# Optimization experiments

Hardware: AMD Instinct MI355X
Metric: run time of the kernel (lower is better)

Reference implementation:

```python
import jax, jax.numpy as jnp
import numpy as np

D_MODEL = 512
NHEAD = 4
HEAD_DIM = D_MODEL // NHEAD


def setup_inputs() -> dict:
    key = jax.random.key(0)
    ks = jax.random.split(key, 12)
    B, S = 2, 4096
    s = 1.0 / np.sqrt(D_MODEL)
    inp = {
        "query": jax.random.normal(ks[0], (B, S, D_MODEL), jnp.float32),
        "key": jax.random.normal(ks[1], (B, S, D_MODEL), jnp.float32),
        "value": jax.random.normal(ks[2], (B, S, D_MODEL), jnp.float32),
        "Wq": jax.random.uniform(ks[3], (D_MODEL, D_MODEL), jnp.float32, -s, s),
        "bq": jax.random.uniform(ks[4], (D_MODEL,), jnp.float32, -s, s),
        "Wk": jax.random.uniform(ks[5], (D_MODEL, D_MODEL), jnp.float32, -s, s),
        "bk": jax.random.uniform(ks[6], (D_MODEL,), jnp.float32, -s, s),
        "Wv": jax.random.uniform(ks[7], (D_MODEL, D_MODEL), jnp.float32, -s, s),
        "bv": jax.random.uniform(ks[8], (D_MODEL,), jnp.float32, -s, s),
        "Wo": jax.random.uniform(ks[9], (D_MODEL, D_MODEL), jnp.float32, -s, s),
        "bo": jax.random.uniform(ks[10], (D_MODEL,), jnp.float32, -s, s),
    }
    return inp


def reference(query, key, value, Wq, bq, Wk, bk, Wv, bv, Wo, bo):
    B, Sq, _ = query.shape
    Sk = key.shape[1]
    # projections (torch Linear: x @ W.T + b); split heads -> [B, H, S, hd]
    def proj(x, W, b, S):
        return (x @ W.T + b).reshape(B, S, NHEAD, HEAD_DIM).transpose(0, 2, 1, 3)
    Q = proj(query, Wq, bq, Sq)
    K = proj(key, Wk, bk, Sk)
    V = proj(value, Wv, bv, Sk)
    scale = 1.0 / np.sqrt(HEAD_DIM).astype(np.float32)
    scores = jnp.einsum("bhqd,bhkd->bhqk", Q, K) * scale  # [B,H,Sq,Sk]
    weights = jax.nn.softmax(scores, axis=-1)
    out = jnp.einsum("bhqk,bhkd->bhqd", weights, V)  # [B,H,Sq,hd]
    out = out.transpose(0, 2, 1, 3).reshape(B, Sq, D_MODEL)
    return out @ Wo.T + bo
```

## Files before the change

### kernel.cpp

```cpp
#include <hip/hip_runtime.h>


#define D_MODEL 512
#define NHEAD 4
#define HD 128
#define S_ 4096

typedef __attribute__((ext_vector_type(8))) short bf16x8;
typedef __attribute__((ext_vector_type(4))) short bf16x4;
typedef __attribute__((ext_vector_type(4))) float f32x4;
typedef __attribute__((ext_vector_type(2))) unsigned uint2v;
typedef __attribute__((ext_vector_type(4))) unsigned uint4v;

#define SCQ (0.08838834764831845f * 1.4426950408889634f)

__device__ __forceinline__ short f2bf(float f) {
    unsigned u = __builtin_bit_cast(unsigned, f);
    u += 0x7fffu + ((u >> 16) & 1u);
    return (short)(u >> 16);
}
__device__ __forceinline__ unsigned pk2bf(float a, float b) {
    unsigned ua = __builtin_bit_cast(unsigned, a);
    ua += 0x7fffu + ((ua >> 16) & 1u);
    unsigned ub = __builtin_bit_cast(unsigned, b);
    ub += 0x7fffu + ((ub >> 16) & 1u);
    return (ua >> 16) | (ub & 0xffff0000u);
}
__device__ __forceinline__ void gl2lds16(const short* g, short* l) {
    __builtin_amdgcn_global_load_lds(
        (const __attribute__((address_space(1))) void*)g,
        (__attribute__((address_space(3))) void*)l, 16, 0, 0);
}

__global__ __launch_bounds__(256) void convert_kernel(
    const float* __restrict__ s0, const float* __restrict__ s1,
    const float* __restrict__ s2, const float* __restrict__ s3,
    const float* __restrict__ s4, const float* __restrict__ s5,
    const float* __restrict__ s6,
    short* __restrict__ d0, short* __restrict__ d1, short* __restrict__ d2,
    short* __restrict__ d3, short* __restrict__ d4, short* __restrict__ d5,
    short* __restrict__ d6)
{
    int seg = blockIdx.y;
    const float* src; short* dst; int n;
    const int NBIG = 2 * S_ * D_MODEL;
    const int NW = D_MODEL * D_MODEL;
    switch (seg) {
        case 0: src = s0; dst = d0; n = NBIG; break;
        case 1: src = s1; dst = d1; n = NBIG; break;
        case 2: src = s2; dst = d2; n = NBIG; break;
        case 3: src = s3; dst = d3; n = NW; break;
        case 4: src = s4; dst = d4; n = NW; break;
        case 5: src = s5; dst = d5; n = NW; break;
        default: src = s6; dst = d6; n = NW; break;
    }
    int idx = (blockIdx.x * 256 + threadIdx.x) * 8;
    if (idx >= n) return;
    float4 a = *(const float4*)(src + idx);
    float4 b = *(const float4*)(src + idx + 4);
    uint4v o;
    o[0] = pk2bf(a.x, a.y); o[1] = pk2bf(a.z, a.w);
    o[2] = pk2bf(b.x, b.y); o[3] = pk2bf(b.z, b.w);
    *(uint4v*)(dst + idx) = o;
}

__global__ __launch_bounds__(256) void qkv_kernel(
    const short* __restrict__ qb, const short* __restrict__ kb,
    const short* __restrict__ vb,
    const short* __restrict__ Wqb, const short* __restrict__ Wkb,
    const short* __restrict__ Wvb,
    const float* __restrict__ bq, const float* __restrict__ bk,
    const float* __restrict__ bv,
    short* __restrict__ Qh, short* __restrict__ Kh, short* __restrict__ VT)
{
    __shared__ short smem[24576];
    int z = blockIdx.z;
    const short* A    = (z == 0) ? qb  : (z == 1) ? kb  : vb;
    const short* W    = (z == 0) ? Wqb : (z == 1) ? Wkb : Wvb;
    const float* bias = (z == 0) ? bq  : (z == 1) ? bk  : bv;
    short* out        = (z == 0) ? Qh  : (z == 1) ? Kh  : VT;
    int vmode = (z == 2);
    float osc = (z == 0) ? SCQ : 1.0f;

    int t = threadIdx.x;
    int wv = t >> 6, ln = t & 63, q4 = ln >> 4, c = ln & 15;
    int m0 = blockIdx.x * 64, n0 = blockIdx.y * 128;
    f32x4 acc[8] = {};

    {
        short* lAd = smem;
        short* lBd = smem + 8192;
        #pragma unroll
        for (int i = 0; i < 2; ++i) {
            int id = i * 256 + t;
            int m = id >> 3, kgp = id & 7;
            gl2lds16(A + (size_t)(m0 + m) * 512 + ((kgp ^ (m & 7)) << 3), &lAd[id * 8]);
        }
        #pragma unroll
        for (int i = 0; i < 4; ++i) {
            int id = i * 256 + t;
            int n = id >> 3, kgp = id & 7;
            gl2lds16(W + (size_t)(n0 + n) * 512 + ((kgp ^ (n & 7)) << 3), &lBd[id * 8]);
        }
    }
    asm volatile("s_waitcnt vmcnt(0)" ::: "memory");
    __builtin_amdgcn_s_barrier();
    __builtin_amdgcn_sched_barrier(0);

    int cur = 0;
    for (int k0 = 0; k0 < 512; k0 += 64) {
        int more = (k0 < 448);
        if (more) {
            short* lAd = smem + (cur ^ 1) * 4096;
            short* lBd = smem + 8192 + (cur ^ 1) * 8192;
            int kn = k0 + 64;
            #pragma unroll
            for (int i = 0; i < 2; ++i) {
                int id = i * 256 + t;
                int m = id >> 3, kgp = id & 7;
                gl2lds16(A + (size_t)(m0 + m) * 512 + kn + ((kgp ^ (m & 7)) << 3), &lAd[id * 8]);
            }
            #pragma unroll
            for (int i = 0; i < 4; ++i) {
                int id = i * 256 + t;
                int n = id >> 3, kgp = id & 7;
                gl2lds16(W + (size_t)(n0 + n) * 512 + kn + ((kgp ^ (n & 7)) << 3), &lBd[id * 8]);
            }
        }
        short* lAc = smem + cur * 4096;
        short* lBc = smem + 8192 + cur * 8192;
        __builtin_amdgcn_s_setprio(1);
        #pragma unroll
        for (int ks = 0; ks < 2; ++ks) {
            int kg = ks * 4 + q4;
            int m = wv * 16 + c;
            bf16x8 af = *(bf16x8*)&lAc[m * 64 + ((kg ^ (m & 7)) << 3)];
            bf16x8 bfr[8];
            #pragma unroll
            for (int nt = 0; nt < 8; ++nt) {
                int n = nt * 16 + c;
                bfr[nt] = *(bf16x8*)&lBc[n * 64 + ((kg ^ (n & 7)) << 3)];
            }
            #pragma unroll
            for (int nt = 0; nt < 8; ++nt)
                acc[nt] = __builtin_amdgcn_mfma_f32_16x16x32_bf16(af, bfr[nt], acc[nt], 0, 0, 0);
        }
        __builtin_amdgcn_s_setprio(0);
        if (more) asm volatile("s_waitcnt vmcnt(0)" ::: "memory");
        __builtin_amdgcn_s_barrier();
        __builtin_amdgcn_sched_barrier(0);
        cur ^= 1;
    }

    if (vmode == 0) {
        const int TS = 136;
        short* lT = smem;
        for (int nt = 0; nt < 8; ++nt) {
            float bv_ = bias[n0 + nt * 16 + c];
            for (int r = 0; r < 4; ++r) {
                int srow = wv * 16 + q4 * 4 + r;
                lT[srow * TS + nt * 16 + c] = f2bf((acc[nt][r] + bv_) * osc);
            }
        }
        __syncthreads();
        int bb = m0 >> 12, sbase = m0 & 4095, h = blockIdx.y;
        for (int i = 0; i < 4; ++i) {
            int id = i * 256 + t;
            int row = id >> 4, g = id & 15;
            bf16x8 vv = *(bf16x8*)&lT[row * TS + g * 8];
            *(bf16x8*)&out[((size_t)((bb * NHEAD + h) * S_ + sbase + row)) * HD + g * 8] = vv;
        }
    } else {
        short* lB0 = smem + 8192;
        for (int nt = 0; nt < 8; ++nt) {
            int d = nt * 16 + c;
            float bv_ = bias[n0 + d];
            uint2v pv;
            pv[0] = pk2bf(acc[nt][0] + bv_, acc[nt][1] + bv_);
            pv[1] = pk2bf(acc[nt][2] + bv_, acc[nt][3] + bv_);
            int gr = wv * 4 + q4;
            *(uint2v*)&lB0[d * 64 + ((gr ^ (d & 15)) << 2)] = pv;
        }
        __syncthreads();
        int bb = m0 >> 12, sbase = m0 & 4095, h = blockIdx.y;
        for (int i = 0; i < 8; ++i) {
            int id = i * 256 + t;
            int d = id >> 4, grl = id & 15;
            bf16x4 v = *(bf16x4*)&lB0[d * 64 + ((grl ^ (d & 15)) << 2)];
            *(bf16x4*)&out[((size_t)((bb * NHEAD + h) * HD + d)) * S_ + sbase + grl * 4] = v;
        }
    }
}

__global__ __launch_bounds__(256) void outproj_kernel(
    const short* __restrict__ A, const short* __restrict__ W,
    const float* __restrict__ bias, float* __restrict__ out)
{
    __shared__ short smem[24576];
    int t = threadIdx.x;
    int wv = t >> 6, ln = t & 63, q4 = ln >> 4, c = ln & 15;
    int m0 = blockIdx.x * 64, n0 = blockIdx.y * 128;
    f32x4 acc[8] = {};

    {
        short* lAd = smem;
        short* lBd = smem + 8192;
        #pragma unroll
        for (int i = 0; i < 2; ++i) {
            int id = i * 256 + t;
            int m = id >> 3, kgp = id & 7;
            gl2lds16(A + (size_t)(m0 + m) * 512 + ((kgp ^ (m & 7)) << 3), &lAd[id * 8]);
        }
        #pragma unroll
        for (int i = 0; i < 4; ++i) {
            int id = i * 256 + t;
            int n = id >> 3, kgp = id & 7;
            gl2lds16(W + (size_t)(n0 + n) * 512 + ((kgp ^ (n & 7)) << 3), &lBd[id * 8]);
        }
    }
    asm volatile("s_waitcnt vmcnt(0)" ::: "memory");
    __builtin_amdgcn_s_barrier();
    __builtin_amdgcn_sched_barrier(0);

    int cur = 0;
    for (int k0 = 0; k0 < 512; k0 += 64) {
        int more = (k0 < 448);
        if (more) {
            short* lAd = smem + (cur ^ 1) * 4096;
            short* lBd = smem + 8192 + (cur ^ 1) * 8192;
            int kn = k0 + 64;
            #pragma unroll
            for (int i = 0; i < 2; ++i) {
                int id = i * 256 + t;
                int m = id >> 3, kgp = id & 7;
                gl2lds16(A + (size_t)(m0 + m) * 512 + kn + ((kgp ^ (m & 7)) << 3), &lAd[id * 8]);
            }
            #pragma unroll
            for (int i = 0; i < 4; ++i) {
                int id = i * 256 + t;
                int n = id >> 3, kgp = id & 7;
                gl2lds16(W + (size_t)(n0 + n) * 512 + kn + ((kgp ^ (n & 7)) << 3), &lBd[id * 8]);
            }
        }
        short* lAc = smem + cur * 4096;
        short* lBc = smem + 8192 + cur * 8192;
        __builtin_amdgcn_s_setprio(1);
        #pragma unroll
        for (int ks = 0; ks < 2; ++ks) {
            int kg = ks * 4 + q4;
            int m = wv * 16 + c;
            bf16x8 af = *(bf16x8*)&lAc[m * 64 + ((kg ^ (m & 7)) << 3)];
            bf16x8 bfr[8];
            #pragma unroll
            for (int nt = 0; nt < 8; ++nt) {
                int n = nt * 16 + c;
                bfr[nt] = *(bf16x8*)&lBc[n * 64 + ((kg ^ (n & 7)) << 3)];
            }
            #pragma unroll
            for (int nt = 0; nt < 8; ++nt)
                acc[nt] = __builtin_amdgcn_mfma_f32_16x16x32_bf16(af, bfr[nt], acc[nt], 0, 0, 0);
        }
        __builtin_amdgcn_s_setprio(0);
        if (more) asm volatile("s_waitcnt vmcnt(0)" ::: "memory");
        __builtin_amdgcn_s_barrier();
        __builtin_amdgcn_sched_barrier(0);
        cur ^= 1;
    }

    for (int nt = 0; nt < 8; ++nt) {
        int col = n0 + nt * 16 + c;
        float bv_ = bias[col];
        for (int r = 0; r < 4; ++r) {
            int mrow = m0 + wv * 16 + q4 * 4 + r;
            out[(size_t)mrow * 512 + col] = acc[nt][r] + bv_;
        }
    }
}

__device__ __forceinline__ void stage_k(const short* __restrict__ Kh, size_t base,
                                        int kk, short* dst, int t) {
    #pragma unroll
    for (int i = 0; i < 4; ++i) {
        int id = i * 256 + t;
        int m = id >> 4, kgp = id & 15;
        gl2lds16(Kh + base + (size_t)(kk + m) * HD + ((kgp ^ (m & 7)) << 3), &dst[id * 8]);
    }
}
__device__ __forceinline__ void stage_vt(const short* __restrict__ VTg, size_t base,
                                         int kk, short* dst, int t) {
    #pragma unroll
    for (int i = 0; i < 4; ++i) {
        int id = i * 256 + t;
        int mv = id >> 3, kgvp = id & 7;
        gl2lds16(VTg + base + (size_t)mv * S_ + kk + ((kgvp ^ (mv & 7)) << 3), &dst[id * 8]);
    }
}
__device__ __forceinline__ void qk_tile(const short* kb, const bf16x8 (&qf)[2][4],
                                        int q4, int c, f32x4 (&sf)[2][4]) {
    #pragma unroll
    for (int ks = 0; ks < 4; ++ks) {
        int kg = ks * 4 + q4;
        bf16x8 af[4];
        #pragma unroll
        for (int kt = 0; kt < 4; ++kt) {
            int row = kt * 16 + c;
            af[kt] = *(bf16x8*)&kb[row * 128 + ((kg ^ (row & 7)) << 3)];
        }
        #pragma unroll
        for (int qt = 0; qt < 2; ++qt)
            #pragma unroll
            for (int kt = 0; kt < 4; ++kt)
                sf[qt][kt] = __builtin_amdgcn_mfma_f32_16x16x32_bf16(
                    af[kt], qf[qt][ks], sf[qt][kt], 0, 0, 0);
    }
}
__device__ __forceinline__ void pv_tile(const short* vb, const bf16x8 (&bp)[2][2],
                                        int q4, int c, f32x4 (&of)[8][2]) {
    #pragma unroll
    for (int ksv = 0; ksv < 2; ++ksv) {
        int kg = ksv * 4 + q4;
        bf16x8 av[8];
        #pragma unroll
        for (int dt = 0; dt < 8; ++dt) {
            int row = dt * 16 + c;
            av[dt] = *(bf16x8*)&vb[row * 64 + ((kg ^ (row & 7)) << 3)];
        }
        #pragma unroll
        for (int qt = 0; qt < 2; ++qt)
            #pragma unroll
            for (int dt = 0; dt < 8; ++dt)
                of[dt][qt] = __builtin_amdgcn_mfma_f32_16x16x32_bf16(
                    av[dt], bp[qt][ksv], of[dt][qt], 0, 0, 0);
    }
}
__device__ __forceinline__ void sm_tile(const f32x4 (&sf)[2][4], float (&lrun)[2],
                                        bf16x8 (&bp)[2][2]) {
    #pragma unroll
    for (int qt = 0; qt < 2; ++qt) {
        unsigned dlo[4], dhi[4];
        float lt = 0.f;
        #pragma unroll
        for (int kt = 0; kt < 4; ++kt) {
            float p0 = exp2f(sf[qt][kt][0]);
            float p1 = exp2f(sf[qt][kt][1]);
            float p2 = exp2f(sf[qt][kt][2]);
            float p3 = exp2f(sf[qt][kt][3]);
            lt += (p0 + p1) + (p2 + p3);
            asm("v_cvt_pk_bf16_f32 %0, %1, %2" : "=v"(dlo[kt]) : "v"(p0), "v"(p1));
            asm("v_cvt_pk_bf16_f32 %0, %1, %2" : "=v"(dhi[kt]) : "v"(p2), "v"(p3));
        }
        lrun[qt] += lt;
        #pragma unroll
        for (int ksv = 0; ksv < 2; ++ksv) {
            unsigned x0 = dlo[2 * ksv], y0 = dlo[2 * ksv + 1];
            unsigned x1 = dhi[2 * ksv], y1 = dhi[2 * ksv + 1];
            asm("v_permlane32_swap_b32 %0, %1" : "+v"(x0), "+v"(y0));
            asm("v_permlane16_swap_b32 %0, %1" : "+v"(x0), "+v"(y0));
            asm("v_permlane32_swap_b32 %0, %1" : "+v"(x1), "+v"(y1));
            asm("v_permlane16_swap_b32 %0, %1" : "+v"(x1), "+v"(y1));
            uint4v u; u[0] = x0; u[1] = x1; u[2] = y0; u[3] = y1;
            bp[qt][ksv] = __builtin_bit_cast(bf16x8, u);
        }
    }
}

#define FLASH_BAR() do { \
    asm volatile("s_waitcnt vmcnt(0)" ::: "memory"); \
    __builtin_amdgcn_s_barrier(); \
    __builtin_amdgcn_sched_barrier(0); } while (0)

__global__ __launch_bounds__(256, 2) void flash_kernel(
    const short* __restrict__ Qh, const short* __restrict__ Kh,
    const short* __restrict__ VTg, short* __restrict__ AO,
    float* __restrict__ U, float* __restrict__ ML, int nsplit, int kkspan)
{
    __shared__ short lK[2][64 * 128];
    __shared__ short lVT[2][128 * 64];
    int t = threadIdx.x;
    int wv = t >> 6, ln = t & 63, q4 = ln >> 4, c = ln & 15;
    int bh = blockIdx.x;
    int s0 = blockIdx.y * 128;
    int z = blockIdx.z;
    const size_t base = (size_t)bh * S_ * HD;

    bf16x8 qf[2][4];
    #pragma unroll
    for (int qt = 0; qt < 2; ++qt) {
        int s = s0 + wv * 32 + qt * 16 + c;
        const short* qp = Qh + base + (size_t)s * HD + q4 * 8;
        #pragma unroll
        for (int ks = 0; ks < 4; ++ks)
            qf[qt][ks] = *(const bf16x8*)(qp + ks * 32);
    }

    f32x4 of[8][2] = {};
    float lrun[2] = {};
    bf16x8 bpA[2][2], bpB[2][2];

    int kkbeg = z * kkspan;
    int ntl = kkspan >> 6;

    stage_k(Kh, base, kkbeg, &lK[0][0], t);
    FLASH_BAR();

    {
        stage_k(Kh, base, kkbeg + 64, &lK[1][0], t);
        stage_vt(VTg, base, kkbeg, &lVT[0][0], t);
        f32x4 sf[2][4] = {};
        __builtin_amdgcn_s_setprio(1);
        qk_tile(&lK[0][0], qf, q4, c, sf);
        __builtin_amdgcn_s_setprio(0);
        sm_tile(sf, lrun, bpA);
        FLASH_BAR();
    }

    for (int j = 1; j + 1 < ntl; j += 2) {
        {
            int kk0 = kkbeg + j * 64;
            stage_k(Kh, base, kk0 + 64, &lK[0][0], t);
            stage_vt(VTg, base, kk0, &lVT[1][0], t);
            f32x4 sf[2][4] = {};
            __builtin_amdgcn_s_setprio(1);
            qk_tile(&lK[1][0], qf, q4, c, sf);
            pv_tile(&lVT[0][0], bpA, q4, c, of);
            __builtin_amdgcn_s_setprio(0);
            sm_tile(sf, lrun, bpB);
            FLASH_BAR();
        }
        {
            int kk0 = kkbeg + (j + 1) * 64;
            if (j + 2 < ntl) stage_k(Kh, base, kk0 + 64, &lK[1][0], t);
            stage_vt(VTg, base, kk0, &lVT[0][0], t);
            f32x4 sf[2][4] = {};
            __builtin_amdgcn_s_setprio(1);
            qk_tile(&lK[0][0], qf, q4, c, sf);
            pv_tile(&lVT[1][0], bpB, q4, c, of);
            __builtin_amdgcn_s_setprio(0);
            sm_tile(sf, lrun, bpA);
            FLASH_BAR();
        }
    }

    {
        int kk0 = kkbeg + (ntl - 1) * 64;
        stage_vt(VTg, base, kk0, &lVT[1][0], t);
        f32x4 sf[2][4] = {};
        __builtin_amdgcn_s_setprio(1);
        qk_tile(&lK[1][0], qf, q4, c, sf);
        pv_tile(&lVT[0][0], bpA, q4, c, of);
        __builtin_amdgcn_s_setprio(0);
        sm_tile(sf, lrun, bpB);
        FLASH_BAR();
    }

    __builtin_amdgcn_s_setprio(1);
    pv_tile(&lVT[1][0], bpB, q4, c, of);
    __builtin_amdgcn_s_setprio(0);

    #pragma unroll
    for (int qt = 0; qt < 2; ++qt) {
        lrun[qt] += __shfl_xor(lrun[qt], 16);
        lrun[qt] += __shfl_xor(lrun[qt], 32);
    }

    if (nsplit > 1) {
        #pragma unroll
        for (int qt = 0; qt < 2; ++qt) {
            int s = s0 + wv * 32 + qt * 16 + c;
            size_t rowu = (size_t)(z * 8 + bh) * S_ + s;
            float* up = U + rowu * HD;
            #pragma unroll
            for (int dt = 0; dt < 8; ++dt)
                *(f32x4*)&up[dt * 16 + q4 * 4] = of[dt][qt];
            if (q4 == 0) ML[rowu] = lrun[qt];
        }
    } else {
        int b = bh >> 2, h = bh & 3;
        #pragma unroll
        for (int qt = 0; qt < 2; ++qt) {
            float inv = 1.0f / lrun[qt];
            int s = s0 + wv * 32 + qt * 16 + c;
            short* dst = AO + ((size_t)(b * S_ + s)) * D_MODEL + h * HD;
            #pragma unroll
            for (int dt = 0; dt < 8; ++dt) {
                uint2v ov;
                ov[0] = pk2bf(of[dt][qt][0] * inv, of[dt][qt][1] * inv);
                ov[1] = pk2bf(of[dt][qt][2] * inv, of[dt][qt][3] * inv);
                *(uint2v*)(dst + dt * 16 + q4 * 4) = ov;
            }
        }
    }
}

__global__ __launch_bounds__(256) void combine_kernel(
    const float* __restrict__ U, const float* __restrict__ ML,
    short* __restrict__ AO, int nsplit)
{
    int row = blockIdx.x * 8 + (threadIdx.x >> 5);
    int d4 = (threadIdx.x & 31) * 4;
    const int R = 8 * S_;
    float l = 0.f;
    f32x4 u = {0.f, 0.f, 0.f, 0.f};
    for (int zz = 0; zz < nsplit; ++zz) {
        l += ML[(size_t)zz * R + row];
        f32x4 uz = *(const f32x4*)&U[((size_t)zz * R + row) * HD + d4];
        u += uz;
    }
    float inv = 1.0f / l;
    uint2v o;
    o[0] = pk2bf(u[0] * inv, u[1] * inv);
    o[1] = pk2bf(u[2] * inv, u[3] * inv);
    int bh = row >> 12, s = row & 4095;
    int b = bh >> 2, h = bh & 3;
    *(uint2v*)&AO[((size_t)(b * S_ + s)) * D_MODEL + h * HD + d4] = o;
}

extern "C" void kernel_launch(void* const* d_in, const int* in_sizes, int n_in,
                              void* d_out, int out_size, void* d_ws, size_t ws_size,
                              hipStream_t stream) {
    const float* q  = (const float*)d_in[0];
    const float* k  = (const float*)d_in[1];
    const float* v  = (const float*)d_in[2];
    const float* Wq = (const float*)d_in[3];
    const float* bq = (const float*)d_in[4];
    const float* Wk = (const float*)d_in[5];
    const float* bk = (const float*)d_in[6];
    const float* Wv = (const float*)d_in[7];
    const float* bv = (const float*)d_in[8];
    const float* Wo = (const float*)d_in[9];
    const float* bo = (const float*)d_in[10];

    const size_t HS = (size_t)2 * NHEAD * S_ * HD;
    const size_t NBIG = HS;
    const size_t NW = (size_t)D_MODEL * D_MODEL;
    const size_t R = (size_t)8 * S_;

    char* wsb = (char*)d_ws;
    short* Qh = (short*)wsb;
    short* Kh = Qh + HS;
    short* VT = Kh + HS;
    short* AO = VT + HS;
    char* r2 = wsb + 4 * HS * 2;
    short* qb  = (short*)r2;
    short* kb  = qb + NBIG;
    short* vb  = kb + NBIG;
    short* Wqb = vb + NBIG;
    short* Wkb = Wqb + NW;
    short* Wvb = Wkb + NW;
    float* U   = (float*)r2;

    int nsplit = 1;
    size_t r2sz = 3 * NBIG * 2 + 3 * NW * 2;
    {
        int cand = 2;
        size_t r2c = (size_t)cand * R * HD * 4;
        if (r2c < 3 * NBIG * 2 + 3 * NW * 2) r2c = 3 * NBIG * 2 + 3 * NW * 2;
        size_t need = 4 * HS * 2 + r2c + (size_t)cand * R * 4 + NW * 2;
        if (ws_size >= need) { nsplit = cand; r2sz = r2c; }
    }
    float* ML  = (float*)(r2 + r2sz);
    short* Wob = (short*)((char*)ML + (size_t)nsplit * R * 4);
    int kkspan = S_ / nsplit;

    dim3 blk(256);
    convert_kernel<<<dim3(2048, 7), blk, 0, stream>>>(
        q, k, v, Wq, Wk, Wv, Wo, qb, kb, vb, Wqb, Wkb, Wvb, Wob);
    qkv_kernel<<<dim3(128, 4, 3), blk, 0, stream>>>(
        qb, kb, vb, Wqb, Wkb, Wvb, bq, bk, bv, Qh, Kh, VT);
    flash_kernel<<<dim3(8, 32, nsplit), blk, 0, stream>>>(
        Qh, Kh, VT, AO, U, ML, nsplit, kkspan);
    if (nsplit > 1)
        combine_kernel<<<dim3(S_), blk, 0, stream>>>(U, ML, AO, nsplit);
    outproj_kernel<<<dim3(128, 4), blk, 0, stream>>>(AO, Wob, bo, (float*)d_out);
}
```

Before: 228.8 us.

## Fuse activation bf16 conversion into QKV GEMM and split-combine into out-projection

The QKV projection now reads fp32 activations directly, converts them to bf16 in registers and writes them into swizzled LDS, so the large activation conversion pass and its intermediate buffers go away; the convert kernel now only handles the weights. The out-projection A-tile fetch now merges the two flash split partials and normalizes them inline, which removes the separate combine kernel and the AO round trip. The cost is that the A loads become register-staged rather than direct global-to-LDS loads, adding VGPR pressure and fp32 traffic inside the GEMMs. The split-combine path also reads twice as many fp32 bytes per A tile and recomputes it for each of the 4 N-blocks.

After: 230.9 us. About the same (+0.9%).

```diff
diff --git a/kernel.cpp b/kernel.cpp
--- a/kernel.cpp
+++ b/kernel.cpp
@@ -26,6 +26,12 @@
     ub += 0x7fffu + ((ub >> 16) & 1u);
     return (ua >> 16) | (ub & 0xffff0000u);
 }
+__device__ __forceinline__ uint4v pk8(float4 a, float4 b) {
+    uint4v o;
+    o[0] = pk2bf(a.x, a.y); o[1] = pk2bf(a.z, a.w);
+    o[2] = pk2bf(b.x, b.y); o[3] = pk2bf(b.z, b.w);
+    return o;
+}
 __device__ __forceinline__ void gl2lds16(const short* g, short* l) {
     __builtin_amdgcn_global_load_lds(
         (const __attribute__((address_space(1))) void*)g,
@@ -35,38 +41,21 @@
 __global__ __launch_bounds__(256) void convert_kernel(
     const float* __restrict__ s0, const float* __restrict__ s1,
     const float* __restrict__ s2, const float* __restrict__ s3,
-    const float* __restrict__ s4, const float* __restrict__ s5,
-    const float* __restrict__ s6,
-    short* __restrict__ d0, short* __restrict__ d1, short* __restrict__ d2,
-    short* __restrict__ d3, short* __restrict__ d4, short* __restrict__ d5,
-    short* __restrict__ d6)
+    short* __restrict__ d0, short* __restrict__ d1,
+    short* __restrict__ d2, short* __restrict__ d3)
 {
     int seg = blockIdx.y;
-    const float* src; short* dst; int n;
-    const int NBIG = 2 * S_ * D_MODEL;
-    const int NW = D_MODEL * D_MODEL;
-    switch (seg) {
-        case 0: src = s0; dst = d0; n = NBIG; break;
-        case 1: src = s1; dst = d1; n = NBIG; break;
-        case 2: src = s2; dst = d2; n = NBIG; break;
-        case 3: src = s3; dst = d3; n = NW; break;
-        case 4: src = s4; dst = d4; n = NW; break;
-        case 5: src = s5; dst = d5; n = NW; break;
-        default: src = s6; dst = d6; n = NW; break;
-    }
+    const float* src = (seg == 0) ? s0 : (seg == 1) ? s1 : (seg == 2) ? s2 : s3;
+    short* dst       = (seg == 0) ? d0 : (seg == 1) ? d1 : (seg == 2) ? d2 : d3;
     int idx = (blockIdx.x * 256 + threadIdx.x) * 8;
-    if (idx >= n) return;
     float4 a = *(const float4*)(src + idx);
     float4 b = *(const float4*)(src + idx + 4);
-    uint4v o;
-    o[0] = pk2bf(a.x, a.y); o[1] = pk2bf(a.z, a.w);
-    o[2] = pk2bf(b.x, b.y); o[3] = pk2bf(b.z, b.w);
-    *(uint4v*)(dst + idx) = o;
+    *(uint4v*)(dst + idx) = pk8(a, b);
 }
 
 __global__ __launch_bounds__(256) void qkv_kernel(
-    const short* __restrict__ qb, const short* __restrict__ kb,
-    const short* __restrict__ vb,
+    const float* __restrict__ qf32, const float* __restrict__ kf32,
+    const float* __restrict__ vf32,
     const short* __restrict__ Wqb, const short* __restrict__ Wkb,
     const short* __restrict__ Wvb,
     const float* __restrict__ bq, const float* __restrict__ bk,
@@ -75,10 +64,10 @@
 {
     __shared__ short smem[24576];
     int z = blockIdx.z;
-    const short* A    = (z == 0) ? qb  : (z == 1) ? kb  : vb;
-    const short* W    = (z == 0) ? Wqb : (z == 1) ? Wkb : Wvb;
-    const float* bias = (z == 0) ? bq  : (z == 1) ? bk  : bv;
-    short* out        = (z == 0) ? Qh  : (z == 1) ? Kh  : VT;
+    const float* A    = (z == 0) ? qf32 : (z == 1) ? kf32 : vf32;
+    const short* W    = (z == 0) ? Wqb  : (z == 1) ? Wkb  : Wvb;
+    const float* bias = (z == 0) ? bq   : (z == 1) ? bk   : bv;
+    short* out        = (z == 0) ? Qh   : (z == 1) ? Kh   : VT;
     int vmode = (z == 2);
     float osc = (z == 0) ? SCQ : 1.0f;
 
@@ -87,15 +76,18 @@
     int m0 = blockIdx.x * 64, n0 = blockIdx.y * 128;
     f32x4 acc[8] = {};
 
+    int mA0 = t >> 3, kg0 = t & 7;
+    int mA1 = 32 + (t >> 3), kg1 = t & 7;
+    const float* a0p = A + (size_t)(m0 + mA0) * 512 + kg0 * 8;
+    const float* a1p = A + (size_t)(m0 + mA1) * 512 + kg1 * 8;
+    int sw0 = mA0 * 64 + ((kg0 ^ (mA0 & 7)) << 3);
+    int sw1 = mA1 * 64 + ((kg1 ^ (mA1 & 7)) << 3);
+    float4 pa00, pa01, pa10, pa11;
+
+    pa00 = *(const float4*)(a0p);     pa01 = *(const float4*)(a0p + 4);
+    pa10 = *(const float4*)(a1p);     pa11 = *(const float4*)(a1p + 4);
     {
-        short* lAd = smem;
         short* lBd = smem + 8192;
-        #pragma unroll
-        for (int i = 0; i < 2; ++i) {
-            int id = i * 256 + t;
-            int m = id >> 3, kgp = id & 7;
-            gl2lds16(A + (size_t)(m0 + m) * 512 + ((kgp ^ (m & 7)) << 3), &lAd[id * 8]);
-        }
         #pragma unroll
         for (int i = 0; i < 4; ++i) {
             int id = i * 256 + t;
@@ -104,6 +96,9 @@
         }
     }
     asm volatile("s_waitcnt vmcnt(0)" ::: "memory");
+    *(uint4v*)&smem[sw0] = pk8(pa00, pa01);
+    *(uint4v*)&smem[sw1] = pk8(pa10, pa11);
+    asm volatile("s_waitcnt lgkmcnt(0)" ::: "memory");
     __builtin_amdgcn_s_barrier();
     __builtin_amdgcn_sched_barrier(0);
 
@@ -111,15 +106,10 @@
     for (int k0 = 0; k0 < 512; k0 += 64) {
         int more = (k0 < 448);
         if (more) {
-            short* lAd = smem + (cur ^ 1) * 4096;
+            int kn = k0 + 64;
+            pa00 = *(const float4*)(a0p + kn); pa01 = *(const float4*)(a0p + kn + 4);
+            pa10 = *(const float4*)(a1p + kn); pa11 = *(const float4*)(a1p + kn + 4);
             short* lBd = smem + 8192 + (cur ^ 1) * 8192;
-            int kn = k0 + 64;
-            #pragma unroll
-            for (int i = 0; i < 2; ++i) {
-                int id = i * 256 + t;
-                int m = id >> 3, kgp = id & 7;
-                gl2lds16(A + (size_t)(m0 + m) * 512 + kn + ((kgp ^ (m & 7)) << 3), &lAd[id * 8]);
-            }
             #pragma unroll
             for (int i = 0; i < 4; ++i) {
                 int id = i * 256 + t;
@@ -146,7 +136,13 @@
                 acc[nt] = __builtin_amdgcn_mfma_f32_16x16x32_bf16(af, bfr[nt], acc[nt], 0, 0, 0);
         }
         __builtin_amdgcn_s_setprio(0);
-        if (more) asm volatile("s_waitcnt vmcnt(0)" ::: "memory");
+        if (more) {
+            asm volatile("s_waitcnt vmcnt(0)" ::: "memory");
+            short* lAd = smem + (cur ^ 1) * 4096;
+            *(uint4v*)&lAd[sw0] = pk8(pa00, pa01);
+            *(uint4v*)&lAd[sw1] = pk8(pa10, pa11);
+        }
+        asm volatile("s_waitcnt lgkmcnt(0)" ::: "memory");
         __builtin_amdgcn_s_barrier();
         __builtin_amdgcn_sched_barrier(0);
         cur ^= 1;
@@ -193,8 +189,9 @@
 }
 
 __global__ __launch_bounds__(256) void outproj_kernel(
-    const short* __restrict__ A, const short* __restrict__ W,
-    const float* __restrict__ bias, float* __restrict__ out)
+    const short* __restrict__ AO, const float* __restrict__ U,
+    const float* __restrict__ ML, const short* __restrict__ W,
+    const float* __restrict__ bias, float* __restrict__ out, int nsplit)
 {
     __shared__ short smem[24576];
     int t = threadIdx.x;
@@ -202,15 +199,42 @@
     int m0 = blockIdx.x * 64, n0 = blockIdx.y * 128;
     f32x4 acc[8] = {};
 
+    int mA0 = t >> 3, kg0 = t & 7;
+    int mA1 = 32 + (t >> 3), kg1 = t & 7;
+    int g0row = m0 + mA0, g1row = m0 + mA1;
+    int b0 = g0row >> 12, s0r = g0row & 4095;
+    int b1 = g1row >> 12, s1r = g1row & 4095;
+    int sw0 = mA0 * 64 + ((kg0 ^ (mA0 & 7)) << 3);
+    int sw1 = mA1 * 64 + ((kg1 ^ (mA1 & 7)) << 3);
+    uint4v va0, va1;
+
+    auto fetchA = [&](int k0, int b, int srow, int kg, uint4v& dst) {
+        if (nsplit > 1) {
+            int bh = b * 4 + (k0 >> 7);
+            size_t r0 = (size_t)bh * S_ + srow;
+            size_t r1 = (size_t)(8 + bh) * S_ + srow;
+            const float* u0 = U + r0 * HD + (k0 & 127) + kg * 8;
+            const float* u1 = U + r1 * HD + (k0 & 127) + kg * 8;
+            float4 x0 = *(const float4*)(u0);
+            float4 x1 = *(const float4*)(u0 + 4);
+            float4 y0 = *(const float4*)(u1);
+            float4 y1 = *(const float4*)(u1 + 4);
+            float inv = 1.0f / (ML[r0] + ML[r1]);
+            uint4v o;
+            o[0] = pk2bf((x0.x + y0.x) * inv, (x0.y + y0.y) * inv);
+            o[1] = pk2bf((x0.z + y0.z) * inv, (x0.w + y0.w) * inv);
+            o[2] = pk2bf((x1.x + y1.x) * inv, (x1.y + y1.y) * inv);
+            o[3] = pk2bf((x1.z + y1.z) * inv, (x1.w + y1.w) * inv);
+            dst = o;
+        } else {
+            dst = *(const uint4v*)(AO + (size_t)(b * S_ + srow) * D_MODEL + k0 + kg * 8);
+        }
+    };
+
+    fetchA(0, b0, s0r, kg0, va0);
+    fetchA(0, b1, s1r, kg1, va1);
     {
-        short* lAd = smem;
         short* lBd = smem + 8192;
-        #pragma unroll
-        for (int i = 0; i < 2; ++i) {
-            int id = i * 256 + t;
-            int m = id >> 3, kgp = id & 7;
-            gl2lds16(A + (size_t)(m0 + m) * 512 + ((kgp ^ (m & 7)) << 3), &lAd[id * 8]);
-        }
         #pragma unroll
         for (int i = 0; i < 4; ++i) {
             int id = i * 256 + t;
@@ -219,6 +243,9 @@
         }
     }
     asm volatile("s_waitcnt vmcnt(0)" ::: "memory");
+    *(uint4v*)&smem[sw0] = va0;
+    *(uint4v*)&smem[sw1] = va1;
+    asm volatile("s_waitcnt lgkmcnt(0)" ::: "memory");
     __builtin_amdgcn_s_barrier();
     __builtin_amdgcn_sched_barrier(0);
 
@@ -226,15 +253,10 @@
     for (int k0 = 0; k0 < 512; k0 += 64) {
         int more = (k0 < 448);
         if (more) {
-            short* lAd = smem + (cur ^ 1) * 4096;
+            int kn = k0 + 64;
+            fetchA(kn, b0, s0r, kg0, va0);
+            fetchA(kn, b1, s1r, kg1, va1);
             short* lBd = smem + 8192 + (cur ^ 1) * 8192;
-            int kn = k0 + 64;
-            #pragma unroll
-            for (int i = 0; i < 2; ++i) {
-                int id = i * 256 + t;
-                int m = id >> 3, kgp = id & 7;
-                gl2lds16(A + (size_t)(m0 + m) * 512 + kn + ((kgp ^ (m & 7)) << 3), &lAd[id * 8]);
-            }
             #pragma unroll
             for (int i = 0; i < 4; ++i) {
                 int id = i * 256 + t;
@@ -261,7 +283,13 @@
                 acc[nt] = __builtin_amdgcn_mfma_f32_16x16x32_bf16(af, bfr[nt], acc[nt], 0, 0, 0);
         }
         __builtin_amdgcn_s_setprio(0);
-        if (more) asm volatile("s_waitcnt vmcnt(0)" ::: "memory");
+        if (more) {
+            asm volatile("s_waitcnt vmcnt(0)" ::: "memory");
+            short* lAd = smem + (cur ^ 1) * 4096;
+            *(uint4v*)&lAd[sw0] = va0;
+            *(uint4v*)&lAd[sw1] = va1;
+        }
+        asm volatile("s_waitcnt lgkmcnt(0)" ::: "memory");
         __builtin_amdgcn_s_barrier();
         __builtin_amdgcn_sched_barrier(0);
         cur ^= 1;
@@ -490,29 +518,6 @@
             }
         }
     }
-}
-
-__global__ __launch_bounds__(256) void combine_kernel(
-    const float* __restrict__ U, const float* __restrict__ ML,
-    short* __restrict__ AO, int nsplit)
-{
-    int row = blockIdx.x * 8 + (threadIdx.x >> 5);
-    int d4 = (threadIdx.x & 31) * 4;
-    const int R = 8 * S_;
-    float l = 0.f;
-    f32x4 u = {0.f, 0.f, 0.f, 0.f};
-    for (int zz = 0; zz < nsplit; ++zz) {
-        l += ML[(size_t)zz * R + row];
-        f32x4 uz = *(const f32x4*)&U[((size_t)zz * R + row) * HD + d4];
-        u += uz;
-    }
-    float inv = 1.0f / l;
-    uint2v o;
-    o[0] = pk2bf(u[0] * inv, u[1] * inv);
-    o[1] = pk2bf(u[2] * inv, u[3] * inv);
-    int bh = row >> 12, s = row & 4095;
-    int b = bh >> 2, h = bh & 3;
-    *(uint2v*)&AO[((size_t)(b * S_ + s)) * D_MODEL + h * HD + d4] = o;
 }
 
 extern "C" void kernel_launch(void* const* d_in, const int* in_sizes, int n_in,
@@ -531,45 +536,33 @@
     const float* bo = (const float*)d_in[10];
 
     const size_t HS = (size_t)2 * NHEAD * S_ * HD;
-    const size_t NBIG = HS;
     const size_t NW = (size_t)D_MODEL * D_MODEL;
     const size_t R = (size_t)8 * S_;
 
-    char* wsb = (char*)d_ws;
-    short* Qh = (short*)wsb;
-    short* Kh = Qh + HS;
-    short* VT = Kh + HS;
-    short* AO = VT + HS;
-    char* r2 = wsb + 4 * HS * 2;
-    short* qb  = (short*)r2;
-    short* kb  = qb + NBIG;
-    short* vb  = kb + NBIG;
-    short* Wqb = vb + NBIG;
+    short* Qh  = (short*)d_ws;
+    short* Kh  = Qh + HS;
+    short* VT  = Kh + HS;
+    short* AO  = VT + HS;
+    short* Wqb = AO + HS;
     short* Wkb = Wqb + NW;
     short* Wvb = Wkb + NW;
-    float* U   = (float*)r2;
+    short* Wob = Wvb + NW;
+    size_t fixed = 4 * HS * 2 + 4 * NW * 2;
 
     int nsplit = 1;
-    size_t r2sz = 3 * NBIG * 2 + 3 * NW * 2;
-    {
-        int cand = 2;
-        size_t r2c = (size_t)cand * R * HD * 4;
-        if (r2c < 3 * NBIG * 2 + 3 * NW * 2) r2c = 3 * NBIG * 2 + 3 * NW * 2;
-        size_t need = 4 * HS * 2 + r2c + (size_t)cand * R * 4 + NW * 2;
-        if (ws_size >= need) { nsplit = cand; r2sz = r2c; }
-    }
-    float* ML  = (float*)(r2 + r2sz);
-    short* Wob = (short*)((char*)ML + (size_t)nsplit * R * 4);
+    size_t need2 = fixed + (size_t)2 * R * HD * 4 + (size_t)2 * R * 4;
+    if (ws_size >= need2) nsplit = 2;
+    float* U  = (float*)((char*)d_ws + fixed);
+    float* ML = (float*)((char*)U + (size_t)nsplit * R * HD * 4);
     int kkspan = S_ / nsplit;
 
     dim3 blk(256);
-    convert_kernel<<<dim3(2048, 7), blk, 0, stream>>>(
-        q, k, v, Wq, Wk, Wv, Wo, qb, kb, vb, Wqb, Wkb, Wvb, Wob);
+    convert_kernel<<<dim3(128, 4), blk, 0, stream>>>(
+        Wq, Wk, Wv, Wo, Wqb, Wkb, Wvb, Wob);
     qkv_kernel<<<dim3(128, 4, 3), blk, 0, stream>>>(
-        qb, kb, vb, Wqb, Wkb, Wvb, bq, bk, bv, Qh, Kh, VT);
+        q, k, v, Wqb, Wkb, Wvb, bq, bk, bv, Qh, Kh, VT);
     flash_kernel<<<dim3(8, 32, nsplit), blk, 0, stream>>>(
         Qh, Kh, VT, AO, U, ML, nsplit, kkspan);
-    if (nsplit > 1)
-        combine_kernel<<<dim3(S_), blk, 0, stream>>>(U, ML, AO, nsplit);
-    outproj_kernel<<<dim3(128, 4), blk, 0, stream>>>(AO, Wob, bo, (float*)d_out);
-}
+    outproj_kernel<<<dim3(128, 4), blk, 0, stream>>>(
+        AO, U, ML, Wob, bo, (float*)d_out, nsplit);
+}
```

## Enlarge QKV projection tile to 128x128 with 2x2 warp layout

Applied to the files above, without the earlier changes.

The QKV GEMM block tile grows from 64x128 to 128x128, with the four warps arranged 2x2 so each computes a 64x64 sub-tile using 4x4 MFMA accumulators. This raises operand reuse per LDS load and halves the number of blocks that reload the weight tiles. The V-transpose epilogue now uses a padded LDS layout and 16-byte stores instead of swizzled 8-byte ones. The costs are more LDS per block (64 KB) and more accumulator registers, and the grid shrinks to 768 blocks, which may lower occupancy.

Result: no change. 229.1 us (+0.2%).

```diff
diff --git a/kernel.cpp b/kernel.cpp
--- a/kernel.cpp
+++ b/kernel.cpp
@@ -73,7 +73,7 @@
     const float* __restrict__ bv,
     short* __restrict__ Qh, short* __restrict__ Kh, short* __restrict__ VT)
 {
-    __shared__ short smem[24576];
+    __shared__ short smem[32768];
     int z = blockIdx.z;
     const short* A    = (z == 0) ? qb  : (z == 1) ? kb  : vb;
     const short* W    = (z == 0) ? Wqb : (z == 1) ? Wkb : Wvb;
@@ -84,23 +84,19 @@
 
     int t = threadIdx.x;
     int wv = t >> 6, ln = t & 63, q4 = ln >> 4, c = ln & 15;
-    int m0 = blockIdx.x * 64, n0 = blockIdx.y * 128;
-    f32x4 acc[8] = {};
+    int wi = wv >> 1, wj = wv & 1;
+    int m0 = blockIdx.x * 128, n0 = blockIdx.y * 128;
+    f32x4 acc[4][4] = {};
 
     {
         short* lAd = smem;
-        short* lBd = smem + 8192;
-        #pragma unroll
-        for (int i = 0; i < 2; ++i) {
+        short* lBd = smem + 16384;
+        #pragma unroll
+        for (int i = 0; i < 4; ++i) {
             int id = i * 256 + t;
             int m = id >> 3, kgp = id & 7;
             gl2lds16(A + (size_t)(m0 + m) * 512 + ((kgp ^ (m & 7)) << 3), &lAd[id * 8]);
-        }
-        #pragma unroll
-        for (int i = 0; i < 4; ++i) {
-            int id = i * 256 + t;
-            int n = id >> 3, kgp = id & 7;
-            gl2lds16(W + (size_t)(n0 + n) * 512 + ((kgp ^ (n & 7)) << 3), &lBd[id * 8]);
+            gl2lds16(W + (size_t)(n0 + m) * 512 + ((kgp ^ (m & 7)) << 3), &lBd[id * 8]);
         }
     }
     asm volatile("s_waitcnt vmcnt(0)" ::: "memory");
@@ -111,39 +107,40 @@
     for (int k0 = 0; k0 < 512; k0 += 64) {
         int more = (k0 < 448);
         if (more) {
-            short* lAd = smem + (cur ^ 1) * 4096;
-            short* lBd = smem + 8192 + (cur ^ 1) * 8192;
+            short* lAd = smem + (cur ^ 1) * 8192;
+            short* lBd = smem + 16384 + (cur ^ 1) * 8192;
             int kn = k0 + 64;
             #pragma unroll
-            for (int i = 0; i < 2; ++i) {
+            for (int i = 0; i < 4; ++i) {
                 int id = i * 256 + t;
                 int m = id >> 3, kgp = id & 7;
                 gl2lds16(A + (size_t)(m0 + m) * 512 + kn + ((kgp ^ (m & 7)) << 3), &lAd[id * 8]);
-            }
-            #pragma unroll
-            for (int i = 0; i < 4; ++i) {
-                int id = i * 256 + t;
-                int n = id >> 3, kgp = id & 7;
-                gl2lds16(W + (size_t)(n0 + n) * 512 + kn + ((kgp ^ (n & 7)) << 3), &lBd[id * 8]);
-            }
-        }
-        short* lAc = smem + cur * 4096;
-        short* lBc = smem + 8192 + cur * 8192;
+                gl2lds16(W + (size_t)(n0 + m) * 512 + kn + ((kgp ^ (m & 7)) << 3), &lBd[id * 8]);
+            }
+        }
+        short* lAc = smem + cur * 8192;
+        short* lBc = smem + 16384 + cur * 8192;
         __builtin_amdgcn_s_setprio(1);
         #pragma unroll
         for (int ks = 0; ks < 2; ++ks) {
             int kg = ks * 4 + q4;
-            int m = wv * 16 + c;
-            bf16x8 af = *(bf16x8*)&lAc[m * 64 + ((kg ^ (m & 7)) << 3)];
-            bf16x8 bfr[8];
-            #pragma unroll
-            for (int nt = 0; nt < 8; ++nt) {
-                int n = nt * 16 + c;
+            bf16x8 af[4], bfr[4];
+            #pragma unroll
+            for (int mt = 0; mt < 4; ++mt) {
+                int m = wi * 64 + mt * 16 + c;
+                af[mt] = *(bf16x8*)&lAc[m * 64 + ((kg ^ (m & 7)) << 3)];
+            }
+            #pragma unroll
+            for (int nt = 0; nt < 4; ++nt) {
+                int n = wj * 64 + nt * 16 + c;
                 bfr[nt] = *(bf16x8*)&lBc[n * 64 + ((kg ^ (n & 7)) << 3)];
             }
             #pragma unroll
-            for (int nt = 0; nt < 8; ++nt)
-                acc[nt] = __builtin_amdgcn_mfma_f32_16x16x32_bf16(af, bfr[nt], acc[nt], 0, 0, 0);
+            for (int mt = 0; mt < 4; ++mt)
+                #pragma unroll
+                for (int nt = 0; nt < 4; ++nt)
+                    acc[mt][nt] = __builtin_amdgcn_mfma_f32_16x16x32_bf16(
+                        af[mt], bfr[nt], acc[mt][nt], 0, 0, 0);
         }
         __builtin_amdgcn_s_setprio(0);
         if (more) asm volatile("s_waitcnt vmcnt(0)" ::: "memory");
@@ -152,42 +149,50 @@
         cur ^= 1;
     }
 
+    const int TS = 136;
+    short* lT = smem;
+    int bb = m0 >> 12, sbase = m0 & 4095, h = blockIdx.y;
     if (vmode == 0) {
-        const int TS = 136;
-        short* lT = smem;
-        for (int nt = 0; nt < 8; ++nt) {
-            float bv_ = bias[n0 + nt * 16 + c];
-            for (int r = 0; r < 4; ++r) {
-                int srow = wv * 16 + q4 * 4 + r;
-                lT[srow * TS + nt * 16 + c] = f2bf((acc[nt][r] + bv_) * osc);
+        #pragma unroll
+        for (int nt = 0; nt < 4; ++nt) {
+            float bv_ = bias[n0 + wj * 64 + nt * 16 + c];
+            #pragma unroll
+            for (int mt = 0; mt < 4; ++mt) {
+                #pragma unroll
+                for (int r = 0; r < 4; ++r) {
+                    int srow = wi * 64 + mt * 16 + q4 * 4 + r;
+                    lT[srow * TS + wj * 64 + nt * 16 + c] =
+                        f2bf((acc[mt][nt][r] + bv_) * osc);
+                }
             }
         }
         __syncthreads();
-        int bb = m0 >> 12, sbase = m0 & 4095, h = blockIdx.y;
-        for (int i = 0; i < 4; ++i) {
+        for (int i = 0; i < 8; ++i) {
             int id = i * 256 + t;
             int row = id >> 4, g = id & 15;
             bf16x8 vv = *(bf16x8*)&lT[row * TS + g * 8];
             *(bf16x8*)&out[((size_t)((bb * NHEAD + h) * S_ + sbase + row)) * HD + g * 8] = vv;
         }
     } else {
-        short* lB0 = smem + 8192;
-        for (int nt = 0; nt < 8; ++nt) {
-            int d = nt * 16 + c;
+        #pragma unroll
+        for (int nt = 0; nt < 4; ++nt) {
+            int d = wj * 64 + nt * 16 + c;
             float bv_ = bias[n0 + d];
-            uint2v pv;
-            pv[0] = pk2bf(acc[nt][0] + bv_, acc[nt][1] + bv_);
-            pv[1] = pk2bf(acc[nt][2] + bv_, acc[nt][3] + bv_);
-            int gr = wv * 4 + q4;
-            *(uint2v*)&lB0[d * 64 + ((gr ^ (d & 15)) << 2)] = pv;
+            #pragma unroll
+            for (int mt = 0; mt < 4; ++mt) {
+                int srel = wi * 64 + mt * 16 + q4 * 4;
+                uint2v pv;
+                pv[0] = pk2bf(acc[mt][nt][0] + bv_, acc[mt][nt][1] + bv_);
+                pv[1] = pk2bf(acc[mt][nt][2] + bv_, acc[mt][nt][3] + bv_);
+                *(uint2v*)&lT[d * TS + srel] = pv;
+            }
         }
         __syncthreads();
-        int bb = m0 >> 12, sbase = m0 & 4095, h = blockIdx.y;
         for (int i = 0; i < 8; ++i) {
             int id = i * 256 + t;
-            int d = id >> 4, grl = id & 15;
-            bf16x4 v = *(bf16x4*)&lB0[d * 64 + ((grl ^ (d & 15)) << 2)];
-            *(bf16x4*)&out[((size_t)((bb * NHEAD + h) * HD + d)) * S_ + sbase + grl * 4] = v;
+            int d = id >> 4, g = id & 15;
+            bf16x8 vv = *(bf16x8*)&lT[d * TS + g * 8];
+            *(bf16x8*)&out[((size_t)((bb * NHEAD + h) * HD + d)) * S_ + sbase + g * 8] = vv;
         }
     }
 }
@@ -565,7 +570,7 @@
     dim3 blk(256);
     convert_kernel<<<dim3(2048, 7), blk, 0, stream>>>(
         q, k, v, Wq, Wk, Wv, Wo, qb, kb, vb, Wqb, Wkb, Wvb, Wob);
-    qkv_kernel<<<dim3(128, 4, 3), blk, 0, stream>>>(
+    qkv_kernel<<<dim3(64, 4, 3), blk, 0, stream>>>(
         qb, kb, vb, Wqb, Wkb, Wvb, bq, bk, bv, Qh, Kh, VT);
     flash_kernel<<<dim3(8, 32, nsplit), blk, 0, stream>>>(
         Qh, Kh, VT, AO, U, ML, nsplit, kkspan);
```
